# Kernel optimization log

Measured on AMD Instinct MI355X. Metric: run time of the kernel, lower is better.

The kernel has to match this reference:

```python
import jax, jax.numpy as jnp
import numpy as np

# SoftmaxMatMulSparse forward: out = softmax(x1, dim=-1) @ x2.
# The masker/sparsify/quantize path only compresses activations saved for
# backward; the forward output is the exact dense softmax-matmul.

def setup_inputs() -> dict:
    key = jax.random.key(0)
    k1, k2 = jax.random.split(key)
    x1 = jax.random.normal(k1, (1, 16, 2048, 2048), dtype=jnp.float32)  # [B,H,S,S] scores
    x2 = jax.random.normal(k2, (1, 16, 2048, 64), dtype=jnp.float32)    # [B,H,S,Dh] values
    return {"x1": x1, "x2": x2}

def reference(x1, x2):
    probs = jax.nn.softmax(x1, axis=-1)          # [B,H,S,S]
    return jnp.matmul(probs, x2)                 # [B,H,S,Dh]
```

## Files before the change

### kernel.cpp

```cpp
#include <hip/hip_runtime.h>
#include <hip/hip_bf16.h>
#include <stdint.h>


#define H_  16
#define S_  2048
#define D_  64
#define QT  128
#define QTF 64
#define KT  128
#define NT  (S_ / KT)

typedef short bf16x8 __attribute__((ext_vector_type(8)));
typedef float f32x4  __attribute__((ext_vector_type(4)));

__device__ __forceinline__ uint16_t f2bf(float f) {
  uint32_t u = __builtin_bit_cast(uint32_t, f);
  u += 0x7fffu + ((u >> 16) & 1u);
  return (uint16_t)(u >> 16);
}

__global__ __launch_bounds__(256) void vtrans_kernel(const float* __restrict__ x2,
                                                     uint16_t* __restrict__ x2t) {
  __shared__ float t[D_][64 + 1];
  const int h  = blockIdx.x >> 5;
  const int k0 = (blockIdx.x & 31) << 6;
  const float* src = x2 + ((size_t)h * S_ + k0) * D_;
#pragma unroll
  for (int p = 0; p < 4; ++p) {
    int flat = p * 1024 + threadIdx.x * 4;
    int k = flat >> 6, d = flat & 63;
    float4 v = *(const float4*)(src + (size_t)k * D_ + d);
    t[d + 0][k] = v.x; t[d + 1][k] = v.y; t[d + 2][k] = v.z; t[d + 3][k] = v.w;
  }
  __syncthreads();
  uint16_t* dst = x2t + (size_t)h * D_ * S_ + k0;
#pragma unroll
  for (int p = 0; p < 4; ++p) {
    int flat = p * 1024 + threadIdx.x * 4;
    int d = flat >> 6, k = flat & 63;
    ushort4 o;
    o.x = f2bf(t[d][k + 0]); o.y = f2bf(t[d][k + 1]);
    o.z = f2bf(t[d][k + 2]); o.w = f2bf(t[d][k + 3]);
    *(ushort4*)(dst + (size_t)d * S_ + k) = o;
  }
}

__global__ __launch_bounds__(512) void smm_q128(const float* __restrict__ x1,
                                                const uint16_t* __restrict__ x2t,
                                                float* __restrict__ out) {
  __shared__ __attribute__((aligned(16))) uint16_t pT[QT][KT];
  __shared__ __attribute__((aligned(16))) uint16_t vT[D_][KT];

  const int bid  = ((int)blockIdx.x & 7) * 32 + ((int)blockIdx.x >> 3);
  const int tid  = threadIdx.x;
  const int lane = tid & 63;
  const int w    = tid >> 6;
  const int h    = bid >> 4;
  const int q0   = (bid & 15) * QT;

  f32x4 acc[4];
  f32x4 accS;
#pragma unroll
  for (int c = 0; c < 4; ++c) acc[c] = (f32x4){0.f, 0.f, 0.f, 0.f};
  accS = (f32x4){0.f, 0.f, 0.f, 0.f};

  bf16x8 ones;
  {
    short v = ((lane & 15) == 0) ? (short)0x3F80 : (short)0;
#pragma unroll
    for (int e = 0; e < 8; ++e) ones[e] = v;
  }

  const float* x1p = x1 + ((size_t)h * S_ + q0) * S_;
  const int prow = tid >> 5;
  const int pk4  = (tid & 31) << 2;
  const int arow = lane & 15;
  const int kgrp = lane >> 4;

  for (int kt = 0; kt < NT; ++kt) {
    __syncthreads();

#pragma unroll
    for (int p = 0; p < 8; ++p) {
      int r = prow + p * 16;
      float4 v = *(const float4*)(x1p + (size_t)r * S_ + kt * KT + pk4);
      uint32_t lo = (uint32_t)f2bf(__expf(v.x)) | ((uint32_t)f2bf(__expf(v.y)) << 16);
      uint32_t hi = (uint32_t)f2bf(__expf(v.z)) | ((uint32_t)f2bf(__expf(v.w)) << 16);
      int byteoff = (pk4 * 2) ^ ((r & 15) << 4);
      *(uint2*)((char*)(&pT[r][0]) + byteoff) = make_uint2(lo, hi);
    }

    {
      const uint16_t* vp = x2t + (size_t)h * D_ * S_ + kt * KT;
#pragma unroll
      for (int p = 0; p < 2; ++p) {
        int flat = p * 512 + tid;
        int dd = flat >> 4;
        int ch = flat & 15;
        uint4 v = *(const uint4*)(vp + (size_t)dd * S_ + ch * 8);
        int byteoff = (ch * 16) ^ ((dd & 15) << 4);
        *(uint4*)((char*)(&vT[dd][0]) + byteoff) = v;
      }
    }
    __syncthreads();

#pragma unroll
    for (int ks = 0; ks < 4; ++ks) {
      int kb = ks * 64 + kgrp * 16;
      int ar = w * 16 + arow;
      bf16x8 a = *(const bf16x8*)((const char*)(&pT[ar][0]) + (kb ^ (arow << 4)));
      accS = __builtin_amdgcn_mfma_f32_16x16x32_bf16(a, ones, accS, 0, 0, 0);
#pragma unroll
      for (int c = 0; c < 4; ++c) {
        int bc = c * 16 + arow;
        bf16x8 b = *(const bf16x8*)((const char*)(&vT[bc][0]) + (kb ^ (arow << 4)));
        acc[c] = __builtin_amdgcn_mfma_f32_16x16x32_bf16(a, b, acc[c], 0, 0, 0);
      }
    }
  }

  float* op = out + ((size_t)h * S_ + q0 + w * 16) * D_;
#pragma unroll
  for (int j = 0; j < 4; ++j) {
    float s = __shfl(accS[j], lane & 48);
    float rs = 1.0f / s;
    int row = (lane >> 4) * 4 + j;
#pragma unroll
    for (int c = 0; c < 4; ++c) {
      op[(size_t)row * D_ + c * 16 + (lane & 15)] = acc[c][j] * rs;
    }
  }
}

__global__ __launch_bounds__(256) void smm_lds(const float* __restrict__ x1,
                                               const float* __restrict__ x2,
                                               float* __restrict__ out) {
  __shared__ __attribute__((aligned(16))) uint16_t pT[QTF][KT];
  __shared__ __attribute__((aligned(16))) uint16_t vT[D_][KT];

  const int tid  = threadIdx.x;
  const int lane = tid & 63;
  const int w    = tid >> 6;
  const int h    = blockIdx.x >> 5;
  const int q0   = (blockIdx.x & 31) * QTF;

  f32x4 acc[4];
  f32x4 accS;
#pragma unroll
  for (int c = 0; c < 4; ++c) acc[c] = (f32x4){0.f, 0.f, 0.f, 0.f};
  accS = (f32x4){0.f, 0.f, 0.f, 0.f};

  bf16x8 ones;
  {
    short v = ((lane & 15) == 0) ? (short)0x3F80 : (short)0;
#pragma unroll
    for (int e = 0; e < 8; ++e) ones[e] = v;
  }

  const float* x1p = x1 + ((size_t)h * S_ + q0) * S_;
  const int prow = tid >> 5;
  const int pk4  = (tid & 31) << 2;
  const int arow = lane & 15;
  const int kgrp = lane >> 4;

  for (int kt = 0; kt < NT; ++kt) {
    __syncthreads();
#pragma unroll
    for (int p = 0; p < 8; ++p) {
      int r = prow + p * 8;
      float4 v = *(const float4*)(x1p + (size_t)r * S_ + kt * KT + pk4);
      uint32_t lo = (uint32_t)f2bf(__expf(v.x)) | ((uint32_t)f2bf(__expf(v.y)) << 16);
      uint32_t hi = (uint32_t)f2bf(__expf(v.z)) | ((uint32_t)f2bf(__expf(v.w)) << 16);
      int byteoff = (pk4 * 2) ^ ((r & 15) << 4);
      *(uint2*)((char*)(&pT[r][0]) + byteoff) = make_uint2(lo, hi);
    }
    {
      int dd = tid & 63;
      int kgq = tid >> 6;
      const float* src = x2 + ((size_t)h * S_ + kt * KT) * D_ + dd;
#pragma unroll
      for (int p = 0; p < 4; ++p) {
        int kb = p * 32 + kgq * 8;
        uint16_t tmp[8];
#pragma unroll
        for (int j = 0; j < 8; ++j) tmp[j] = f2bf(src[(size_t)(kb + j) * D_]);
        int byteoff = (kb * 2) ^ ((dd & 15) << 4);
        *(uint4*)((char*)(&vT[dd][0]) + byteoff) = *(uint4*)tmp;
      }
    }
    __syncthreads();
#pragma unroll
    for (int ks = 0; ks < 4; ++ks) {
      int kb = ks * 64 + kgrp * 16;
      int ar = w * 16 + arow;
      bf16x8 a = *(const bf16x8*)((const char*)(&pT[ar][0]) + (kb ^ (arow << 4)));
      accS = __builtin_amdgcn_mfma_f32_16x16x32_bf16(a, ones, accS, 0, 0, 0);
#pragma unroll
      for (int c = 0; c < 4; ++c) {
        int bc = c * 16 + arow;
        bf16x8 b = *(const bf16x8*)((const char*)(&vT[bc][0]) + (kb ^ (arow << 4)));
        acc[c] = __builtin_amdgcn_mfma_f32_16x16x32_bf16(a, b, acc[c], 0, 0, 0);
      }
    }
  }

  float* op = out + ((size_t)h * S_ + q0 + w * 16) * D_;
#pragma unroll
  for (int j = 0; j < 4; ++j) {
    float s = __shfl(accS[j], lane & 48);
    float rs = 1.0f / s;
    int row = (lane >> 4) * 4 + j;
#pragma unroll
    for (int c = 0; c < 4; ++c) {
      op[(size_t)row * D_ + c * 16 + (lane & 15)] = acc[c][j] * rs;
    }
  }
}

extern "C" void kernel_launch(void* const* d_in, const int* in_sizes, int n_in,
                              void* d_out, int out_size, void* d_ws, size_t ws_size,
                              hipStream_t stream) {
  const float* x1 = (const float*)d_in[0];
  const float* x2 = (const float*)d_in[1];
  float* out      = (float*)d_out;
  uint16_t* x2t   = (uint16_t*)d_ws;

  const size_t need = (size_t)H_ * D_ * S_ * sizeof(uint16_t);
  if (ws_size >= need) {
    vtrans_kernel<<<dim3(H_ * (S_ / 64)), dim3(256), 0, stream>>>(x2, x2t);
    smm_q128<<<dim3(H_ * (S_ / QT)), dim3(512), 0, stream>>>(x1, x2t, out);
  } else {
    smm_lds<<<dim3(H_ * (S_ / QTF)), dim3(256), 0, stream>>>(x1, x2, out);
  }
}
```

Before: 75.84 us.

## Shrink main kernel to 64-row tiles and use nontemporal loads and stores

Replaces the 128-query-row, 512-thread block (with XCD-aware block remapping) by a 64-row, 256-thread block, which doubles the grid to 512 blocks. It also switches the streaming x1 reads, the x2 reads in the transpose kernel and the output writes to nontemporal loads and stores. The goal is better occupancy and less cache pollution from the 256 MB score stream. In exchange, each block reloads the V tile for half as many rows, and the block swizzle is dropped.

```diff
diff --git a/kernel.cpp b/kernel.cpp
--- a/kernel.cpp
+++ b/kernel.cpp
@@ -6,9 +6,8 @@
 #define H_  16
 #define S_  2048
 #define D_  64
-#define QT  128
-#define QTF 64
 #define KT  128
+#define QT  64
 #define NT  (S_ / KT)
 
 typedef short bf16x8 __attribute__((ext_vector_type(8)));
@@ -30,8 +29,8 @@
   for (int p = 0; p < 4; ++p) {
     int flat = p * 1024 + threadIdx.x * 4;
     int k = flat >> 6, d = flat & 63;
-    float4 v = *(const float4*)(src + (size_t)k * D_ + d);
-    t[d + 0][k] = v.x; t[d + 1][k] = v.y; t[d + 2][k] = v.z; t[d + 3][k] = v.w;
+    f32x4 v = __builtin_nontemporal_load((const f32x4*)(src + (size_t)k * D_ + d));
+    t[d + 0][k] = v[0]; t[d + 1][k] = v[1]; t[d + 2][k] = v[2]; t[d + 3][k] = v[3];
   }
   __syncthreads();
   uint16_t* dst = x2t + (size_t)h * D_ * S_ + k0;
@@ -46,18 +45,17 @@
   }
 }
 
-__global__ __launch_bounds__(512) void smm_q128(const float* __restrict__ x1,
-                                                const uint16_t* __restrict__ x2t,
-                                                float* __restrict__ out) {
+__global__ __launch_bounds__(256) void smm_kernel(const float* __restrict__ x1,
+                                                  const uint16_t* __restrict__ x2t,
+                                                  float* __restrict__ out) {
   __shared__ __attribute__((aligned(16))) uint16_t pT[QT][KT];
   __shared__ __attribute__((aligned(16))) uint16_t vT[D_][KT];
 
-  const int bid  = ((int)blockIdx.x & 7) * 32 + ((int)blockIdx.x >> 3);
   const int tid  = threadIdx.x;
   const int lane = tid & 63;
   const int w    = tid >> 6;
-  const int h    = bid >> 4;
-  const int q0   = (bid & 15) * QT;
+  const int h    = blockIdx.x >> 5;
+  const int q0   = (blockIdx.x & 31) * QT;
 
   f32x4 acc[4];
   f32x4 accS;
@@ -83,10 +81,11 @@
 
 #pragma unroll
     for (int p = 0; p < 8; ++p) {
-      int r = prow + p * 16;
-      float4 v = *(const float4*)(x1p + (size_t)r * S_ + kt * KT + pk4);
-      uint32_t lo = (uint32_t)f2bf(__expf(v.x)) | ((uint32_t)f2bf(__expf(v.y)) << 16);
-      uint32_t hi = (uint32_t)f2bf(__expf(v.z)) | ((uint32_t)f2bf(__expf(v.w)) << 16);
+      int r = prow + p * 8;
+      f32x4 v = __builtin_nontemporal_load(
+          (const f32x4*)(x1p + (size_t)r * S_ + kt * KT + pk4));
+      uint32_t lo = (uint32_t)f2bf(__expf(v[0])) | ((uint32_t)f2bf(__expf(v[1])) << 16);
+      uint32_t hi = (uint32_t)f2bf(__expf(v[2])) | ((uint32_t)f2bf(__expf(v[3])) << 16);
       int byteoff = (pk4 * 2) ^ ((r & 15) << 4);
       *(uint2*)((char*)(&pT[r][0]) + byteoff) = make_uint2(lo, hi);
     }
@@ -94,8 +93,8 @@
     {
       const uint16_t* vp = x2t + (size_t)h * D_ * S_ + kt * KT;
 #pragma unroll
-      for (int p = 0; p < 2; ++p) {
-        int flat = p * 512 + tid;
+      for (int p = 0; p < 4; ++p) {
+        int flat = p * 256 + tid;
         int dd = flat >> 4;
         int ch = flat & 15;
         uint4 v = *(const uint4*)(vp + (size_t)dd * S_ + ch * 8);
@@ -128,7 +127,8 @@
     int row = (lane >> 4) * 4 + j;
 #pragma unroll
     for (int c = 0; c < 4; ++c) {
-      op[(size_t)row * D_ + c * 16 + (lane & 15)] = acc[c][j] * rs;
+      float o = acc[c][j] * rs;
+      __builtin_nontemporal_store(o, op + (size_t)row * D_ + c * 16 + (lane & 15));
     }
   }
 }
@@ -136,14 +136,14 @@
 __global__ __launch_bounds__(256) void smm_lds(const float* __restrict__ x1,
                                                const float* __restrict__ x2,
                                                float* __restrict__ out) {
-  __shared__ __attribute__((aligned(16))) uint16_t pT[QTF][KT];
+  __shared__ __attribute__((aligned(16))) uint16_t pT[QT][KT];
   __shared__ __attribute__((aligned(16))) uint16_t vT[D_][KT];
 
   const int tid  = threadIdx.x;
   const int lane = tid & 63;
   const int w    = tid >> 6;
   const int h    = blockIdx.x >> 5;
-  const int q0   = (blockIdx.x & 31) * QTF;
+  const int q0   = (blockIdx.x & 31) * QT;
 
   f32x4 acc[4];
   f32x4 accS;
@@ -229,8 +229,8 @@
   const size_t need = (size_t)H_ * D_ * S_ * sizeof(uint16_t);
   if (ws_size >= need) {
     vtrans_kernel<<<dim3(H_ * (S_ / 64)), dim3(256), 0, stream>>>(x2, x2t);
-    smm_q128<<<dim3(H_ * (S_ / QT)), dim3(512), 0, stream>>>(x1, x2t, out);
+    smm_kernel<<<dim3(H_ * (S_ / QT)), dim3(256), 0, stream>>>(x1, x2t, out);
   } else {
-    smm_lds<<<dim3(H_ * (S_ / QTF)), dim3(256), 0, stream>>>(x1, x2, out);
-  }
-}
+    smm_lds<<<dim3(H_ * (S_ / QT)), dim3(256), 0, stream>>>(x1, x2, out);
+  }
+}
```

Result: slower. 114.9 us (+51.5%).
